# Kernel tuning notes

Measured on AMD Instinct MI355X. Metric: run time of the kernel, lower is better.

## Reference

```python
import jax, jax.numpy as jnp
import numpy as np

N_NODES = 100000
IN_FEAT = 256
OUT_FEAT = 128
N_EDGES = 3200000


def setup_inputs() -> dict:
    key = jax.random.key(0)
    k1, k2, k3, k4, k5 = jax.random.split(key, 5)
    inputs = jax.random.normal(k1, (N_NODES, IN_FEAT), dtype=jnp.float32)
    # xavier-uniform-like init for weight
    limit = float(np.sqrt(6.0 / (IN_FEAT + OUT_FEAT)))
    weight = jax.random.uniform(k2, (IN_FEAT, OUT_FEAT), dtype=jnp.float32, minval=-limit, maxval=limit)
    adj_rows = jnp.sort(jax.random.randint(k3, (N_EDGES,), 0, N_NODES, dtype=jnp.int64))
    adj_cols = jax.random.randint(k4, (N_EDGES,), 0, N_NODES, dtype=jnp.int64)
    adj_vals = jax.random.uniform(k5, (N_EDGES,), dtype=jnp.float32)
    return {"inputs": inputs, "weight": weight, "adj_rows": adj_rows,
            "adj_cols": adj_cols, "adj_vals": adj_vals}


def reference(inputs, weight, adj_rows, adj_cols, adj_vals):
    # support = X @ W  -> [N, out_features]
    support = jnp.matmul(inputs, weight)
    # output = spmm(A, support): out[r] += vals[e] * support[cols[e]] for row r = rows[e]
    gathered = adj_vals[:, None] * support[adj_cols]  # [E, out_features]
    output = jax.ops.segment_sum(gathered, adj_rows, num_segments=N_NODES)
    return output
```

## Files before the change

kernel.cpp:

```cpp
#include <hip/hip_runtime.h>

#define IN_FEAT 256
#define OUT_FEAT 128

typedef __attribute__((ext_vector_type(8))) short bf16x8;
typedef __attribute__((ext_vector_type(4))) float f32x4;

static __device__ __forceinline__ unsigned short f2bf(float f) {
    union { float f; unsigned u; } v; v.f = f;
    unsigned u = v.u;
    return (unsigned short)((u + 0x7FFFu + ((u >> 16) & 1u)) >> 16);
}
static __device__ __forceinline__ float bfl(unsigned u) {
    union { unsigned u; float f; } x; x.u = u << 16; return x.f;
}
static __device__ __forceinline__ float bfh(unsigned u) {
    union { unsigned u; float f; } x; x.u = u & 0xFFFF0000u; return x.f;
}

__global__ __launch_bounds__(256) void prep_wt(const float* __restrict__ W,
                                               unsigned short* __restrict__ Wt) {
    int idx = blockIdx.x * 256 + threadIdx.x;
    int n = idx >> 8, k = idx & 255;
    Wt[idx] = f2bf(W[(size_t)k * OUT_FEAT + n]);
}

__global__ __launch_bounds__(256) void rowptr_kernel(const int* __restrict__ rows,
                                                     int* __restrict__ row_ptr,
                                                     int E, int N) {
    int i = blockIdx.x * 256 + threadIdx.x;
    if (i > N) return;
    int lo = 0, hi = E;
    while (lo < hi) {
        int mid = (lo + hi) >> 1;
        if (rows[mid] < i) lo = mid + 1; else hi = mid;
    }
    row_ptr[i] = lo;
}

__global__ __launch_bounds__(512, 4) void gemm_v3(const float* __restrict__ X,
                                                  const unsigned short* __restrict__ Wt,
                                                  unsigned short* __restrict__ S, int M) {
    __shared__ unsigned short Bs[128 * 256];

    for (int i = threadIdx.x; i < 4096; i += 512) {
        int r = i >> 5, s = i & 31;
        ((uint4*)Bs)[(r << 5) | (s ^ (r & 7))] = ((const uint4*)Wt)[i];
    }
    __syncthreads();

    const int w = threadIdx.x >> 6;
    const int lane = threadIdx.x & 63;
    const int lr = lane & 15, lg = lane >> 4;
    const int m0 = blockIdx.x * 128;
    const int row = m0 + w * 16 + lr;
    const int crow = (row < M) ? row : (M - 1);
    const float4* xp = (const float4*)(X + (size_t)crow * IN_FEAT) + lg * 2;

    f32x4 acc[8];
#pragma unroll
    for (int ni = 0; ni < 8; ++ni) acc[ni] = (f32x4){0.f, 0.f, 0.f, 0.f};

#pragma unroll
    for (int kb = 0; kb < 8; ++kb) {
        float4 f0 = xp[kb * 8];
        float4 f1 = xp[kb * 8 + 1];
        union { uint4 u; bf16x8 v; } a;
        a.u.x = (unsigned)f2bf(f0.x) | ((unsigned)f2bf(f0.y) << 16);
        a.u.y = (unsigned)f2bf(f0.z) | ((unsigned)f2bf(f0.w) << 16);
        a.u.z = (unsigned)f2bf(f1.x) | ((unsigned)f2bf(f1.y) << 16);
        a.u.w = (unsigned)f2bf(f1.z) | ((unsigned)f2bf(f1.w) << 16);
        const int sb = kb * 4 + lg;
#pragma unroll
        for (int ni = 0; ni < 8; ++ni) {
            int r2 = ni * 16 + lr;
            bf16x8 b = ((const bf16x8*)Bs)[(r2 << 5) | (sb ^ (r2 & 7))];
            acc[ni] = __builtin_amdgcn_mfma_f32_16x16x32_bf16(a.v, b, acc[ni], 0, 0, 0);
        }
    }

    __syncthreads();
    unsigned short* Cs = Bs + w * 16 * 128;
#pragma unroll
    for (int ni = 0; ni < 8; ++ni)
#pragma unroll
        for (int j = 0; j < 4; ++j)
            Cs[(lg * 4 + j) * 128 + ni * 16 + lr] = f2bf(acc[ni][j]);
    __syncthreads();

    const int rows_blk = (M - m0 < 128) ? (M - m0) : 128;
    for (int i = threadIdx.x; i < 2048; i += 512) {
        int R = i >> 4;
        if (R < rows_blk)
            ((uint4*)(S + (size_t)(m0 + R) * OUT_FEAT))[i & 15] = ((const uint4*)Bs)[i];
    }
}

__global__ __launch_bounds__(256) void spmm_bf16(const int* __restrict__ cols,
                                                 const float* __restrict__ vals,
                                                 const unsigned short* __restrict__ S,
                                                 const int* __restrict__ row_ptr,
                                                 float* __restrict__ out, int N) {
    const int w = threadIdx.x >> 6;
    const int lane = threadIdx.x & 63;
    const int r = blockIdx.x * 4 + w;
    if (r >= N) return;
    const int g = lane >> 4;
    const int fb = lane & 15;
    const int start = row_ptr[r], end = row_ptr[r + 1];

    float acc[8] = {0.f, 0.f, 0.f, 0.f, 0.f, 0.f, 0.f, 0.f};
    const unsigned short* Sb = S + fb * 8;

    for (int base = start; base < end; base += 16) {
        int   c[4]; float v[4]; uint4 p[4];
#pragma unroll
        for (int u = 0; u < 4; ++u) {
            int e = base + u * 4 + g;
            int ec = (e < end) ? e : (end - 1);
            c[u] = cols[ec];
            v[u] = (e < end) ? vals[ec] : 0.f;
        }
#pragma unroll
        for (int u = 0; u < 4; ++u)
            p[u] = *(const uint4*)(Sb + (size_t)c[u] * OUT_FEAT);
#pragma unroll
        for (int u = 0; u < 4; ++u) {
            float v0 = v[u];
            acc[0] += v0 * bfl(p[u].x); acc[1] += v0 * bfh(p[u].x);
            acc[2] += v0 * bfl(p[u].y); acc[3] += v0 * bfh(p[u].y);
            acc[4] += v0 * bfl(p[u].z); acc[5] += v0 * bfh(p[u].z);
            acc[6] += v0 * bfl(p[u].w); acc[7] += v0 * bfh(p[u].w);
        }
    }

#pragma unroll
    for (int j = 0; j < 8; ++j) {
        acc[j] += __shfl_xor(acc[j], 16);
        acc[j] += __shfl_xor(acc[j], 32);
    }
    if (g == 0) {
        *(float4*)(out + (size_t)r * OUT_FEAT + fb * 8) =
            make_float4(acc[0], acc[1], acc[2], acc[3]);
        *(float4*)(out + (size_t)r * OUT_FEAT + fb * 8 + 4) =
            make_float4(acc[4], acc[5], acc[6], acc[7]);
    }
}

extern "C" void kernel_launch(void* const* d_in, const int* in_sizes, int n_in,
                              void* d_out, int out_size, void* d_ws, size_t ws_size,
                              hipStream_t stream) {
    const float* X    = (const float*)d_in[0];
    const float* W    = (const float*)d_in[1];
    const int*   rows = (const int*)d_in[2];
    const int*   cols = (const int*)d_in[3];
    const float* vals = (const float*)d_in[4];
    float*       out  = (float*)d_out;

    const int M = in_sizes[0] / IN_FEAT;
    const int E = in_sizes[2];

    unsigned short* S  = (unsigned short*)d_ws;
    unsigned short* Wt = S + (size_t)M * OUT_FEAT;
    int* row_ptr = (int*)(Wt + IN_FEAT * OUT_FEAT);

    prep_wt<<<(IN_FEAT * OUT_FEAT) / 256, 256, 0, stream>>>(W, Wt);
    rowptr_kernel<<<(M + 256) / 256 + 1, 256, 0, stream>>>(rows, row_ptr, E, M);
    gemm_v3<<<(M + 127) / 128, 512, 0, stream>>>(X, Wt, S, M);
    spmm_bf16<<<(M + 3) / 4, 256, 0, stream>>>(cols, vals, S, row_ptr, out, M);
}
```

Measured before the change: 310.0 us.

## Split GEMM weight staging into K halves and map SpMM rows to half-waves

The GEMM loads the transposed weight into shared memory in two K halves, halving LDS use per block to allow more resident blocks at the cost of an extra sync round. The SpMM assigns one row per 32-lane half-wavefront, eight rows per block, and processes 8 edges per iteration with an __any-controlled loop. This is meant to cut idle lanes for low-degree rows and raise parallelism, at the cost of more iterations per row and possible divergence between half-waves.

```diff
diff --git a/kernel.cpp b/kernel.cpp
--- a/kernel.cpp
+++ b/kernel.cpp
@@ -38,19 +38,14 @@
     row_ptr[i] = lo;
 }
 
-__global__ __launch_bounds__(512, 4) void gemm_v3(const float* __restrict__ X,
+__global__ __launch_bounds__(512, 4) void gemm_v4(const float* __restrict__ X,
                                                   const unsigned short* __restrict__ Wt,
                                                   unsigned short* __restrict__ S, int M) {
-    __shared__ unsigned short Bs[128 * 256];
+    __shared__ unsigned short Bs[128 * 128];
 
-    for (int i = threadIdx.x; i < 4096; i += 512) {
-        int r = i >> 5, s = i & 31;
-        ((uint4*)Bs)[(r << 5) | (s ^ (r & 7))] = ((const uint4*)Wt)[i];
-    }
-    __syncthreads();
-
-    const int w = threadIdx.x >> 6;
-    const int lane = threadIdx.x & 63;
+    const int t = threadIdx.x;
+    const int w = t >> 6;
+    const int lane = t & 63;
     const int lr = lane & 15, lg = lane >> 4;
     const int m0 = blockIdx.x * 128;
     const int row = m0 + w * 16 + lr;
@@ -61,21 +56,31 @@
 #pragma unroll
     for (int ni = 0; ni < 8; ++ni) acc[ni] = (f32x4){0.f, 0.f, 0.f, 0.f};
 
+#pragma unroll 1
+    for (int h = 0; h < 2; ++h) {
+        __syncthreads();
+        for (int i = t; i < 2048; i += 512) {
+            int r = i >> 4, s = i & 15;
+            ((uint4*)Bs)[(r << 4) | (s ^ (r & 7))] = ((const uint4*)Wt)[r * 32 + h * 16 + s];
+        }
+        __syncthreads();
+
 #pragma unroll
-    for (int kb = 0; kb < 8; ++kb) {
-        float4 f0 = xp[kb * 8];
-        float4 f1 = xp[kb * 8 + 1];
-        union { uint4 u; bf16x8 v; } a;
-        a.u.x = (unsigned)f2bf(f0.x) | ((unsigned)f2bf(f0.y) << 16);
-        a.u.y = (unsigned)f2bf(f0.z) | ((unsigned)f2bf(f0.w) << 16);
-        a.u.z = (unsigned)f2bf(f1.x) | ((unsigned)f2bf(f1.y) << 16);
-        a.u.w = (unsigned)f2bf(f1.z) | ((unsigned)f2bf(f1.w) << 16);
-        const int sb = kb * 4 + lg;
+        for (int kb = 0; kb < 4; ++kb) {
+            float4 f0 = xp[h * 32 + kb * 8];
+            float4 f1 = xp[h * 32 + kb * 8 + 1];
+            union { uint4 u; bf16x8 v; } a;
+            a.u.x = (unsigned)f2bf(f0.x) | ((unsigned)f2bf(f0.y) << 16);
+            a.u.y = (unsigned)f2bf(f0.z) | ((unsigned)f2bf(f0.w) << 16);
+            a.u.z = (unsigned)f2bf(f1.x) | ((unsigned)f2bf(f1.y) << 16);
+            a.u.w = (unsigned)f2bf(f1.z) | ((unsigned)f2bf(f1.w) << 16);
+            const int sb = kb * 4 + lg;
 #pragma unroll
-        for (int ni = 0; ni < 8; ++ni) {
-            int r2 = ni * 16 + lr;
-            bf16x8 b = ((const bf16x8*)Bs)[(r2 << 5) | (sb ^ (r2 & 7))];
-            acc[ni] = __builtin_amdgcn_mfma_f32_16x16x32_bf16(a.v, b, acc[ni], 0, 0, 0);
+            for (int ni = 0; ni < 8; ++ni) {
+                int r2 = ni * 16 + lr;
+                bf16x8 b = ((const bf16x8*)Bs)[(r2 << 4) | (sb ^ (r2 & 7))];
+                acc[ni] = __builtin_amdgcn_mfma_f32_16x16x32_bf16(a.v, b, acc[ni], 0, 0, 0);
+            }
         }
     }
 
@@ -89,37 +94,43 @@
     __syncthreads();
 
     const int rows_blk = (M - m0 < 128) ? (M - m0) : 128;
-    for (int i = threadIdx.x; i < 2048; i += 512) {
+    for (int i = t; i < 2048; i += 512) {
         int R = i >> 4;
         if (R < rows_blk)
             ((uint4*)(S + (size_t)(m0 + R) * OUT_FEAT))[i & 15] = ((const uint4*)Bs)[i];
     }
 }
 
-__global__ __launch_bounds__(256) void spmm_bf16(const int* __restrict__ cols,
-                                                 const float* __restrict__ vals,
-                                                 const unsigned short* __restrict__ S,
-                                                 const int* __restrict__ row_ptr,
-                                                 float* __restrict__ out, int N) {
+__global__ __launch_bounds__(256) void spmm_v4(const int* __restrict__ cols,
+                                               const float* __restrict__ vals,
+                                               const unsigned short* __restrict__ S,
+                                               const int* __restrict__ row_ptr,
+                                               float* __restrict__ out, int N) {
     const int w = threadIdx.x >> 6;
     const int lane = threadIdx.x & 63;
-    const int r = blockIdx.x * 4 + w;
+    const int half = lane >> 5;
+    const int hl = lane & 31;
+    const int g = hl >> 4;
+    const int fb = hl & 15;
+    const int r = blockIdx.x * 8 + w * 2 + half;
     if (r >= N) return;
-    const int g = lane >> 4;
-    const int fb = lane & 15;
-    const int start = row_ptr[r], end = row_ptr[r + 1];
+
+    const int start = row_ptr[r];
+    const int end   = row_ptr[r + 1];
+    const int deg   = end - start;
 
     float acc[8] = {0.f, 0.f, 0.f, 0.f, 0.f, 0.f, 0.f, 0.f};
     const unsigned short* Sb = S + fb * 8;
 
-    for (int base = start; base < end; base += 16) {
-        int   c[4]; float v[4]; uint4 p[4];
+    for (int off = 0; __any(off < deg); off += 8) {
+        int c[4]; float v[4]; uint4 p[4];
 #pragma unroll
         for (int u = 0; u < 4; ++u) {
-            int e = base + u * 4 + g;
-            int ec = (e < end) ? e : (end - 1);
+            int e = start + off + u * 2 + g;
+            bool ok = (e < end);
+            int ec = ok ? e : 0;
             c[u] = cols[ec];
-            v[u] = (e < end) ? vals[ec] : 0.f;
+            v[u] = ok ? vals[ec] : 0.f;
         }
 #pragma unroll
         for (int u = 0; u < 4; ++u)
@@ -135,10 +146,9 @@
     }
 
 #pragma unroll
-    for (int j = 0; j < 8; ++j) {
+    for (int j = 0; j < 8; ++j)
         acc[j] += __shfl_xor(acc[j], 16);
-        acc[j] += __shfl_xor(acc[j], 32);
-    }
+
     if (g == 0) {
         *(float4*)(out + (size_t)r * OUT_FEAT + fb * 8) =
             make_float4(acc[0], acc[1], acc[2], acc[3]);
@@ -166,6 +176,6 @@
 
     prep_wt<<<(IN_FEAT * OUT_FEAT) / 256, 256, 0, stream>>>(W, Wt);
     rowptr_kernel<<<(M + 256) / 256 + 1, 256, 0, stream>>>(rows, row_ptr, E, M);
-    gemm_v3<<<(M + 127) / 128, 512, 0, stream>>>(X, Wt, S, M);
-    spmm_bf16<<<(M + 3) / 4, 256, 0, stream>>>(cols, vals, S, row_ptr, out, M);
+    gemm_v4<<<(M + 127) / 128, 512, 0, stream>>>(X, Wt, S, M);
+    spmm_v4<<<(M + 7) / 8, 256, 0, stream>>>(cols, vals, S, row_ptr, out, M);
 }
```

Measured after the change: 314.0 us. About the same (+1.3%).
